# Kernel tuning notes

Measured on AMD Instinct MI355X. Metric: run time of the kernel, lower is better.

Reference implementation:

```python
import jax, jax.numpy as jnp
import numpy as np

N_NODES = 100000

def gcn_conv(x, W, b, src, dst, norm, n):
    # PyG GCNConv: h = x @ W, then normalized sum-aggregation at target nodes, + bias
    h = x @ W                                   # [N, out]
    msg = h[src] * norm[:, None]                # gather + scale, [E, out]
    out = jax.ops.segment_sum(msg, dst, num_segments=n)
    return out + b

def build_norm(src, dst, n):
    # symmetric normalization with unit edge weights (gcn_norm)
    deg = jax.ops.segment_sum(jnp.ones(src.shape[0], jnp.float32), dst, num_segments=n)
    dinv = jnp.where(deg > 0, jax.lax.rsqrt(jnp.maximum(deg, 1.0)), 0.0)
    return dinv[src] * dinv[dst]

def setup_inputs() -> dict:
    key = jax.random.key(0)
    ks = jax.random.split(key, 10)
    n, e, din, dout = N_NODES, 1600000, 256, 86
    x = jax.random.normal(ks[0], (n, din), jnp.float32)
    edge_index = jax.random.randint(ks[1], (2, e), 0, n, jnp.int64)
    def glorot(k, i, o):
        s = jnp.sqrt(6.0 / (i + o))
        return jax.random.uniform(k, (i, o), jnp.float32, -s, s)
    return {
        'x': x, 'edge_index': edge_index,
        'W1': glorot(ks[2], din, 128), 'b1': jnp.zeros((128,), jnp.float32),
        'W2': glorot(ks[3], 128, 64),  'b2': jnp.zeros((64,), jnp.float32),
        'W3': glorot(ks[4], 64, 32),   'b3': jnp.zeros((32,), jnp.float32),
        'Wc': glorot(ks[5], 32, dout), 'bc': jnp.zeros((dout,), jnp.float32),
    }

def reference(x, edge_index, W1, b1, W2, b2, W3, b3, Wc, bc):
    n = x.shape[0]
    # add self-loops (GCNConv default add_self_loops=True)
    loops = jnp.arange(n, dtype=edge_index.dtype)
    src = jnp.concatenate([edge_index[0], loops])
    dst = jnp.concatenate([edge_index[1], loops])
    norm = build_norm(src, dst, n)
    h = jnp.tanh(gcn_conv(x, W1, b1, src, dst, norm, n))
    h = jnp.tanh(gcn_conv(h, W2, b2, src, dst, norm, n))
    h = jnp.tanh(gcn_conv(h, W3, b3, src, dst, norm, n))
    out = h @ Wc + bc
    return (out, h)
```

## Files before the change

### kernel.cpp

```cpp
#include <hip/hip_runtime.h>
#include <hip/hip_bf16.h>
#include <hip/hip_fp16.h>


__global__ void count_kernel(const int* __restrict__ dst, int* __restrict__ count, int E) {
    int e = blockIdx.x * blockDim.x + threadIdx.x;
    if (e < E) atomicAdd(&count[dst[e]], 1);
}

__global__ void scan1_kernel(const int* __restrict__ count, int* __restrict__ incl,
                             float* __restrict__ dinv, int* __restrict__ blocksum, int n) {
    __shared__ int lds[1024];
    int t = threadIdx.x;
    int i = blockIdx.x * 1024 + t;
    int v = (i < n) ? count[i] : 0;
    if (i < n) dinv[i] = rsqrtf((float)(v + 1));
    lds[t] = v;
    __syncthreads();
    for (int off = 1; off < 1024; off <<= 1) {
        int add = (t >= off) ? lds[t - off] : 0;
        __syncthreads();
        lds[t] += add;
        __syncthreads();
    }
    if (i < n) incl[i] = lds[t];
    if (t == 1023) blocksum[blockIdx.x] = lds[1023];
}

__global__ void scan2_kernel(const int* __restrict__ blocksum, int* __restrict__ blockoff,
                             int* __restrict__ rowptr, int nb, int n, int E) {
    __shared__ int lds[1024];
    int t = threadIdx.x;
    int v = (t < nb) ? blocksum[t] : 0;
    lds[t] = v;
    __syncthreads();
    for (int off = 1; off < 1024; off <<= 1) {
        int add = (t >= off) ? lds[t - off] : 0;
        __syncthreads();
        lds[t] += add;
        __syncthreads();
    }
    if (t < nb) blockoff[t] = lds[t] - v;
    if (t == 0) rowptr[n] = E;
}

__global__ void scan3_kernel(int* __restrict__ rowptr, const int* __restrict__ count,
                             const int* __restrict__ blockoff, int n) {
    int i = blockIdx.x * blockDim.x + threadIdx.x;
    if (i < n) rowptr[i] = rowptr[i] - count[i] + blockoff[i >> 10];
}

__global__ void scatter_kernel(const int* __restrict__ src, const int* __restrict__ dst,
                               const int* __restrict__ rowptr, int* __restrict__ cursor,
                               int* __restrict__ esrc, int E) {
    int e = blockIdx.x * blockDim.x + threadIdx.x;
    if (e < E) {
        int d = dst[e];
        int pos = rowptr[d] + atomicAdd(&cursor[d], 1);
        esrc[pos] = src[e];
    }
}

template<int DIN, int DOUT, int QN, int BM>
__global__ __launch_bounds__(128) void matmul_scale_kernel(
        const float* __restrict__ X, const float* __restrict__ W,
        const float* __restrict__ dinv, __half* __restrict__ G, int n) {
    constexpr int TM = 8;
    constexpr int NCG = DOUT / (4 * QN);
    constexpr int NRG = BM / TM;
    static_assert(NCG * NRG == 128, "block must be 128 threads");
    constexpr int BK = 32;
    constexpr int XS = BM + 4;

    __shared__ float Xt[BK][XS];
    __shared__ float Ws[BK][DOUT];

    int tid = threadIdx.x;
    int tx = tid % NCG;
    int ty = tid / NCG;
    int row0 = blockIdx.x * BM;

    float acc[TM][4 * QN];
    #pragma unroll
    for (int r = 0; r < TM; r++)
        #pragma unroll
        for (int c = 0; c < 4 * QN; c++) acc[r][c] = 0.f;

    for (int k0 = 0; k0 < DIN; k0 += BK) {
        #pragma unroll
        for (int i = tid; i < BM * (BK / 4); i += 128) {
            int r  = i >> 3;
            int c4 = (i & 7) << 2;
            int rg = row0 + r;
            float4 v = make_float4(0.f, 0.f, 0.f, 0.f);
            if (rg < n) v = *(const float4*)&X[(size_t)rg * DIN + k0 + c4];
            int rs = r ^ ((i & 3) << 3);
            Xt[c4 + 0][rs] = v.x;
            Xt[c4 + 1][rs] = v.y;
            Xt[c4 + 2][rs] = v.z;
            Xt[c4 + 3][rs] = v.w;
        }
        #pragma unroll
        for (int i = tid; i < BK * (DOUT / 4); i += 128) {
            int r  = i / (DOUT / 4);
            int c4 = (i % (DOUT / 4)) << 2;
            *(float4*)&Ws[r][c4] = *(const float4*)&W[(size_t)(k0 + r) * DOUT + c4];
        }
        __syncthreads();

        #pragma unroll 4
        for (int k = 0; k < BK; k++) {
            int rr = (ty * TM) ^ (((k >> 2) & 3) << 3);
            float xv[TM];
            *(float4*)&xv[0] = *(const float4*)&Xt[k][rr];
            *(float4*)&xv[4] = *(const float4*)&Xt[k][rr + 4];
            float wv[4 * QN];
            #pragma unroll
            for (int q = 0; q < QN; q++)
                *(float4*)&wv[q * 4] = *(const float4*)&Ws[k][(tx + q * NCG) * 4];
            #pragma unroll
            for (int r = 0; r < TM; r++)
                #pragma unroll
                for (int c = 0; c < 4 * QN; c++)
                    acc[r][c] += xv[r] * wv[c];
        }
        __syncthreads();
    }

    #pragma unroll
    for (int r = 0; r < TM; r++) {
        int rg = row0 + ty * TM + r;
        if (rg < n) {
            float di = dinv[rg];
            #pragma unroll
            for (int q = 0; q < QN; q++) {
                __half2 p0 = __floats2half2_rn(acc[r][q * 4 + 0] * di, acc[r][q * 4 + 1] * di);
                __half2 p1 = __floats2half2_rn(acc[r][q * 4 + 2] * di, acc[r][q * 4 + 3] * di);
                uint2 w;
                w.x = *reinterpret_cast<unsigned int*>(&p0);
                w.y = *reinterpret_cast<unsigned int*>(&p1);
                *(uint2*)&G[(size_t)rg * DOUT + (tx + q * NCG) * 4] = w;
            }
        }
    }
}

template<int DOUT>
__global__ void agg_kernel(const __half* __restrict__ g, const float* __restrict__ dinv,
                           const int* __restrict__ rowptr, const int* __restrict__ esrc,
                           const float* __restrict__ bias, float* __restrict__ out, int n) {
    constexpr int LPN = DOUT / 4;
    constexpr int NPW = 64 / LPN;
    int wave = threadIdx.x >> 6;
    int lane = threadIdx.x & 63;
    int sub  = lane / LPN;
    int cl   = lane % LPN;
    int node = (blockIdx.x * (blockDim.x >> 6) + wave) * NPW + sub;
    if (node >= n) return;

    const uint2* g2 = (const uint2*)g;
    auto fetch = [&](int s, float4& a) {
        uint2 v = g2[(size_t)s * LPN + cl];
        __half2 h0 = *reinterpret_cast<__half2*>(&v.x);
        __half2 h1 = *reinterpret_cast<__half2*>(&v.y);
        float2 f0 = __half22float2(h0);
        float2 f1 = __half22float2(h1);
        a.x += f0.x; a.y += f0.y; a.z += f1.x; a.w += f1.y;
    };

    float4 acc = make_float4(0.f, 0.f, 0.f, 0.f);
    fetch(node, acc);

    int e = rowptr[node], end = rowptr[node + 1];
    for (; e + 4 <= end; e += 4) {
        int s0 = esrc[e], s1 = esrc[e + 1], s2 = esrc[e + 2], s3 = esrc[e + 3];
        fetch(s0, acc); fetch(s1, acc); fetch(s2, acc); fetch(s3, acc);
    }
    for (; e < end; e++) fetch(esrc[e], acc);

    float di = dinv[node];
    float4 b = *(const float4*)&bias[cl * 4];
    float4 o;
    o.x = tanhf(di * acc.x + b.x);
    o.y = tanhf(di * acc.y + b.y);
    o.z = tanhf(di * acc.z + b.z);
    o.w = tanhf(di * acc.w + b.w);
    *(float4*)&out[(size_t)node * DOUT + cl * 4] = o;
}

__global__ __launch_bounds__(256) void cls_kernel(
        const float* __restrict__ H, const float* __restrict__ Wc,
        const float* __restrict__ bc, float* __restrict__ out, int n) {
    constexpr int DIN = 32, DOUT = 86, RPB = 64;
    __shared__ float Hs[RPB][DIN + 4];
    __shared__ float Ws[DIN][DOUT];
    __shared__ float bs[DOUT];
    int tid = threadIdx.x;
    int row0 = blockIdx.x * RPB;
    for (int i = tid; i < DIN * DOUT; i += 256) Ws[i / DOUT][i % DOUT] = Wc[i];
    if (tid < DOUT) bs[tid] = bc[tid];
    for (int i = tid; i < RPB * (DIN / 4); i += 256) {
        int r = i >> 3, c4 = (i & 7) << 2;
        int rg = row0 + r;
        float4 v = make_float4(0.f, 0.f, 0.f, 0.f);
        if (rg < n) v = *(const float4*)&H[(size_t)rg * DIN + c4];
        *(float4*)&Hs[r][c4] = v;
    }
    __syncthreads();
    for (int idx = tid; idx < RPB * DOUT; idx += 256) {
        int r = idx / DOUT, c = idx - r * DOUT;
        float a = bs[c];
        #pragma unroll
        for (int k = 0; k < DIN; k++) a += Hs[r][k] * Ws[k][c];
        int rg = row0 + r;
        if (rg < n) out[(size_t)rg * DOUT + c] = a;
    }
}

extern "C" void kernel_launch(void* const* d_in, const int* in_sizes, int n_in,
                              void* d_out, int out_size, void* d_ws, size_t ws_size,
                              hipStream_t stream) {
    const float* x  = (const float*)d_in[0];
    const int*   ei = (const int*)d_in[1];
    const float* W1 = (const float*)d_in[2];
    const float* b1 = (const float*)d_in[3];
    const float* W2 = (const float*)d_in[4];
    const float* b2 = (const float*)d_in[5];
    const float* W3 = (const float*)d_in[6];
    const float* b3 = (const float*)d_in[7];
    const float* Wc = (const float*)d_in[8];
    const float* bc = (const float*)d_in[9];

    const int n = in_sizes[0] / 256;
    const int E = in_sizes[1] / 2;
    const int* src = ei;
    const int* dst = ei + E;

    char* ws = (char*)d_ws;
    size_t off = 0;
    auto alloc = [&](size_t bytes) {
        void* p = ws + off;
        off = (off + bytes + 255) & ~(size_t)255;
        return p;
    };
    float*  dinv    = (float*)alloc((size_t)n * 4);
    int*    count   = (int*)  alloc((size_t)n * 4);
    int*    rowptr  = (int*)  alloc((size_t)(n + 1) * 4);
    int*    cursor  = (int*)  alloc((size_t)n * 4);
    int*    blocksum= (int*)  alloc(1024 * 4);
    int*    blockoff= (int*)  alloc(1024 * 4);
    int*    esrc    = (int*)  alloc((size_t)E * 4);
    __half* Gh      = (__half*)alloc((size_t)n * 128 * 2);
    float*  Hf      = (float*)alloc((size_t)n * 128 * 4);

    float* outp = (float*)d_out;
    float* h3   = outp + (size_t)n * 86;

    hipMemsetAsync(count, 0, (size_t)n * 4, stream);
    hipMemsetAsync(cursor, 0, (size_t)n * 4, stream);

    int eblocks = (E + 255) / 256;
    count_kernel<<<eblocks, 256, 0, stream>>>(dst, count, E);
    int nb = (n + 1023) / 1024;
    scan1_kernel<<<nb, 1024, 0, stream>>>(count, rowptr, dinv, blocksum, n);
    scan2_kernel<<<1, 1024, 0, stream>>>(blocksum, blockoff, rowptr, nb, n, E);
    scan3_kernel<<<(n + 255) / 256, 256, 0, stream>>>(rowptr, count, blockoff, n);
    scatter_kernel<<<eblocks, 256, 0, stream>>>(src, dst, rowptr, cursor, esrc, E);

    matmul_scale_kernel<256, 128, 2, 64><<<(n + 63) / 64, 128, 0, stream>>>(x, W1, dinv, Gh, n);
    agg_kernel<128><<<(n + 7) / 8, 256, 0, stream>>>(Gh, dinv, rowptr, esrc, b1, Hf, n);
    matmul_scale_kernel<128, 64, 1, 64><<<(n + 63) / 64, 128, 0, stream>>>(Hf, W2, dinv, Gh, n);
    agg_kernel<64><<<(n + 15) / 16, 256, 0, stream>>>(Gh, dinv, rowptr, esrc, b2, Hf, n);
    matmul_scale_kernel<64, 32, 1, 128><<<(n + 127) / 128, 128, 0, stream>>>(Hf, W3, dinv, Gh, n);
    agg_kernel<32><<<(n + 31) / 32, 256, 0, stream>>>(Gh, dinv, rowptr, esrc, b3, h3, n);
    cls_kernel<<<(n + 63) / 64, 256, 0, stream>>>(h3, Wc, bc, outp, n);
}
```

Measured before the change: 682.7 us.

## Replace FP32 SIMT GEMMs with FP16 MFMA matrix-core GEMM kernel

Replaces the scalar FP32 register-tiled matmul kernels for the three GCN layers with a 256-thread MFMA kernel using the 16x16x32 f16 instruction. Inputs and weights are converted to fp16 while being staged into LDS, and accumulation stays in fp32. The aim is to cut the dense GEMM cost, mostly the 256->128 layer. In exchange, inputs are rounded to fp16 before the multiply, and the epilogue writes scalar fp16 elements instead of vectorized stores, which may reduce store efficiency.

```diff
diff --git a/kernel.cpp b/kernel.cpp
--- a/kernel.cpp
+++ b/kernel.cpp
@@ -1,6 +1,11 @@
 #include <hip/hip_runtime.h>
 #include <hip/hip_bf16.h>
 #include <hip/hip_fp16.h>
+
+typedef _Float16 f16;
+typedef f16 f16x4 __attribute__((ext_vector_type(4)));
+typedef f16 f16x8 __attribute__((ext_vector_type(8)));
+typedef float f32x4 __attribute__((ext_vector_type(4)));
 
 
 __global__ void count_kernel(const int* __restrict__ dst, int* __restrict__ count, int E) {
@@ -61,85 +66,94 @@
     }
 }
 
-template<int DIN, int DOUT, int QN, int BM>
-__global__ __launch_bounds__(128) void matmul_scale_kernel(
+template<int DIN, int DOUT, int WAVES_M>
+__global__ __launch_bounds__(256) void mfma_gemm_kernel(
         const float* __restrict__ X, const float* __restrict__ W,
-        const float* __restrict__ dinv, __half* __restrict__ G, int n) {
-    constexpr int TM = 8;
-    constexpr int NCG = DOUT / (4 * QN);
-    constexpr int NRG = BM / TM;
-    static_assert(NCG * NRG == 128, "block must be 128 threads");
+        const float* __restrict__ dinv, f16* __restrict__ G, int n) {
+    constexpr int WAVES_N = 4 / WAVES_M;
+    constexpr int BM = WAVES_M * 64;
+    constexpr int WN = DOUT / WAVES_N;
+    constexpr int RF = 4;
+    constexpr int CF = WN / 16;
     constexpr int BK = 32;
-    constexpr int XS = BM + 4;
-
-    __shared__ float Xt[BK][XS];
-    __shared__ float Ws[BK][DOUT];
-
-    int tid = threadIdx.x;
-    int tx = tid % NCG;
-    int ty = tid / NCG;
+    constexpr int LDK = BK + 8;
+    constexpr int KPT = BK * DOUT / 256;
+
+    __shared__ f16 As[BM][LDK];
+    __shared__ f16 Bs[DOUT][LDK];
+
+    int tid  = threadIdx.x;
+    int lane = tid & 63;
+    int w    = tid >> 6;
+    int wy   = w / WAVES_N;
+    int wx   = w % WAVES_N;
     int row0 = blockIdx.x * BM;
-
-    float acc[TM][4 * QN];
+    int l15  = lane & 15;
+    int kq   = lane >> 4;
+
+    f32x4 acc[RF][CF];
     #pragma unroll
-    for (int r = 0; r < TM; r++)
-        #pragma unroll
-        for (int c = 0; c < 4 * QN; c++) acc[r][c] = 0.f;
+    for (int i = 0; i < RF; i++)
+        #pragma unroll
+        for (int j = 0; j < CF; j++)
+            acc[i][j] = (f32x4){0.f, 0.f, 0.f, 0.f};
 
     for (int k0 = 0; k0 < DIN; k0 += BK) {
         #pragma unroll
-        for (int i = tid; i < BM * (BK / 4); i += 128) {
+        for (int i = tid; i < BM * 8; i += 256) {
             int r  = i >> 3;
             int c4 = (i & 7) << 2;
             int rg = row0 + r;
             float4 v = make_float4(0.f, 0.f, 0.f, 0.f);
             if (rg < n) v = *(const float4*)&X[(size_t)rg * DIN + k0 + c4];
-            int rs = r ^ ((i & 3) << 3);
-            Xt[c4 + 0][rs] = v.x;
-            Xt[c4 + 1][rs] = v.y;
-            Xt[c4 + 2][rs] = v.z;
-            Xt[c4 + 3][rs] = v.w;
+            f16x4 h = { (f16)v.x, (f16)v.y, (f16)v.z, (f16)v.w };
+            *(f16x4*)&As[r][c4] = h;
         }
-        #pragma unroll
-        for (int i = tid; i < BK * (DOUT / 4); i += 128) {
-            int r  = i / (DOUT / 4);
-            int c4 = (i % (DOUT / 4)) << 2;
-            *(float4*)&Ws[r][c4] = *(const float4*)&W[(size_t)(k0 + r) * DOUT + c4];
+        {
+            int nc = tid % DOUT;
+            int kb = (tid / DOUT) * KPT;
+            f16 tmp[KPT];
+            #pragma unroll
+            for (int j = 0; j < KPT; j++)
+                tmp[j] = (f16)W[(size_t)(k0 + kb + j) * DOUT + nc];
+            if constexpr (KPT == 16) {
+                *(f16x8*)&Bs[nc][kb]     = *(f16x8*)&tmp[0];
+                *(f16x8*)&Bs[nc][kb + 8] = *(f16x8*)&tmp[8];
+            } else if constexpr (KPT == 8) {
+                *(f16x8*)&Bs[nc][kb]     = *(f16x8*)&tmp[0];
+            } else {
+                *(f16x4*)&Bs[nc][kb]     = *(f16x4*)&tmp[0];
+            }
         }
         __syncthreads();
 
-        #pragma unroll 4
-        for (int k = 0; k < BK; k++) {
-            int rr = (ty * TM) ^ (((k >> 2) & 3) << 3);
-            float xv[TM];
-            *(float4*)&xv[0] = *(const float4*)&Xt[k][rr];
-            *(float4*)&xv[4] = *(const float4*)&Xt[k][rr + 4];
-            float wv[4 * QN];
+        f16x8 a[RF], b[CF];
+        #pragma unroll
+        for (int i = 0; i < RF; i++)
+            a[i] = *(f16x8*)&As[wy * 64 + i * 16 + l15][kq * 8];
+        #pragma unroll
+        for (int j = 0; j < CF; j++)
+            b[j] = *(f16x8*)&Bs[wx * WN + j * 16 + l15][kq * 8];
+        #pragma unroll
+        for (int i = 0; i < RF; i++)
             #pragma unroll
-            for (int q = 0; q < QN; q++)
-                *(float4*)&wv[q * 4] = *(const float4*)&Ws[k][(tx + q * NCG) * 4];
-            #pragma unroll
-            for (int r = 0; r < TM; r++)
+            for (int j = 0; j < CF; j++)
+                acc[i][j] = __builtin_amdgcn_mfma_f32_16x16x32_f16(a[i], b[j], acc[i][j], 0, 0, 0);
+        __syncthreads();
+    }
+
+    #pragma unroll
+    for (int i = 0; i < RF; i++) {
+        #pragma unroll
+        for (int r = 0; r < 4; r++) {
+            int row = row0 + wy * 64 + i * 16 + (lane >> 4) * 4 + r;
+            if (row < n) {
+                float di = dinv[row];
                 #pragma unroll
-                for (int c = 0; c < 4 * QN; c++)
-                    acc[r][c] += xv[r] * wv[c];
-        }
-        __syncthreads();
-    }
-
-    #pragma unroll
-    for (int r = 0; r < TM; r++) {
-        int rg = row0 + ty * TM + r;
-        if (rg < n) {
-            float di = dinv[rg];
-            #pragma unroll
-            for (int q = 0; q < QN; q++) {
-                __half2 p0 = __floats2half2_rn(acc[r][q * 4 + 0] * di, acc[r][q * 4 + 1] * di);
-                __half2 p1 = __floats2half2_rn(acc[r][q * 4 + 2] * di, acc[r][q * 4 + 3] * di);
-                uint2 w;
-                w.x = *reinterpret_cast<unsigned int*>(&p0);
-                w.y = *reinterpret_cast<unsigned int*>(&p1);
-                *(uint2*)&G[(size_t)rg * DOUT + (tx + q * NCG) * 4] = w;
+                for (int j = 0; j < CF; j++) {
+                    int col = wx * WN + j * 16 + l15;
+                    G[(size_t)row * DOUT + col] = (f16)(acc[i][j][r] * di);
+                }
             }
         }
     }
@@ -267,11 +281,11 @@
     scan3_kernel<<<(n + 255) / 256, 256, 0, stream>>>(rowptr, count, blockoff, n);
     scatter_kernel<<<eblocks, 256, 0, stream>>>(src, dst, rowptr, cursor, esrc, E);
 
-    matmul_scale_kernel<256, 128, 2, 64><<<(n + 63) / 64, 128, 0, stream>>>(x, W1, dinv, Gh, n);
+    mfma_gemm_kernel<256, 128, 2><<<(n + 127) / 128, 256, 0, stream>>>(x, W1, dinv, (f16*)Gh, n);
     agg_kernel<128><<<(n + 7) / 8, 256, 0, stream>>>(Gh, dinv, rowptr, esrc, b1, Hf, n);
-    matmul_scale_kernel<128, 64, 1, 64><<<(n + 63) / 64, 128, 0, stream>>>(Hf, W2, dinv, Gh, n);
+    mfma_gemm_kernel<128, 64, 4><<<(n + 255) / 256, 256, 0, stream>>>(Hf, W2, dinv, (f16*)Gh, n);
     agg_kernel<64><<<(n + 15) / 16, 256, 0, stream>>>(Gh, dinv, rowptr, esrc, b2, Hf, n);
-    matmul_scale_kernel<64, 32, 1, 128><<<(n + 127) / 128, 128, 0, stream>>>(Hf, W3, dinv, Gh, n);
+    mfma_gemm_kernel<64, 32, 4><<<(n + 255) / 256, 256, 0, stream>>>(Hf, W3, dinv, (f16*)Gh, n);
     agg_kernel<32><<<(n + 31) / 32, 256, 0, stream>>>(Gh, dinv, rowptr, esrc, b3, h3, n);
     cls_kernel<<<(n + 63) / 64, 256, 0, stream>>>(h3, Wc, bc, outp, n);
 }
```

Result: faster. 580.9 us (-14.9%).
